# Performance work log

Hardware: AMD Instinct MI355X
Metric: run time of the kernel (lower is better)

Reference implementation:

```python
import jax, jax.numpy as jnp
import numpy as np

DIN = 1024
DOUT = 1024
NUM_HEAD = 16
HEAD_DIM = DIN // NUM_HEAD  # 64
SEQ = 2048
BS = 4


def setup_inputs() -> dict:
    key = jax.random.key(0)
    ks = jax.random.split(key, 9)
    s_in = 1.0 / np.sqrt(DIN)
    s_out = 1.0 / np.sqrt(DOUT)
    return {
        "x": jax.random.normal(ks[0], (BS, SEQ, DIN), dtype=jnp.float32),
        "Wq": jax.random.normal(ks[1], (DIN, DOUT), dtype=jnp.float32) * s_in,
        "bq": jax.random.normal(ks[2], (DOUT,), dtype=jnp.float32) * s_in,
        "Wk": jax.random.normal(ks[3], (DIN, DOUT), dtype=jnp.float32) * s_in,
        "bk": jax.random.normal(ks[4], (DOUT,), dtype=jnp.float32) * s_in,
        "Wv": jax.random.normal(ks[5], (DIN, DOUT), dtype=jnp.float32) * s_in,
        "bv": jax.random.normal(ks[6], (DOUT,), dtype=jnp.float32) * s_in,
        "Wo": jax.random.normal(ks[7], (DOUT, DOUT), dtype=jnp.float32) * s_out,
        "bo": jax.random.normal(ks[8], (DOUT,), dtype=jnp.float32) * s_out,
    }


def reference(x, Wq, bq, Wk, bk, Wv, bv, Wo, bo):
    bs, n, _ = x.shape
    # projections -> [bs, n, H, hd] -> [bs, H, n, hd]
    def split_heads(t):
        return t.reshape(bs, n, NUM_HEAD, HEAD_DIM).transpose(0, 2, 1, 3)

    q = split_heads(x @ Wq + bq)
    k = split_heads(x @ Wk + bk)
    v = split_heads(x @ Wv + bv)

    # full [bs, H, n, n] scores, causal mask, scaled softmax
    scores = jnp.einsum("bhqd,bhkd->bhqk", q, k)
    causal = jnp.tril(jnp.ones((n, n), dtype=bool))
    scores = jnp.where(causal, scores, -jnp.inf)
    att = jax.nn.softmax(scores / np.sqrt(HEAD_DIM), axis=-1)

    ctx = jnp.einsum("bhqk,bhkd->bhqd", att, v)
    ctx = ctx.transpose(0, 2, 1, 3).reshape(bs, n, DOUT)
    return ctx @ Wo + bo
```

## Files before the change

kernel.cpp:

```cpp
#include <hip/hip_runtime.h>
#include <hip/hip_bf16.h>
#include <stdint.h>

#define DIN   1024
#define DOUT  1024
#define NHEAD 16
#define HDIM  64
#define SEQL  2048
#define BSZ   4
#define MTOT  (BSZ*SEQL)
#define KDIM  1024

typedef __bf16 bf16x8 __attribute__((ext_vector_type(8)));
typedef float  f32x4  __attribute__((ext_vector_type(4)));

__device__ __forceinline__ f32x4 mfma16(bf16x8 a, bf16x8 b, f32x4 c) {
    return __builtin_amdgcn_mfma_f32_16x16x32_bf16(a, b, c, 0, 0, 0);
}

__device__ __forceinline__ void gl_lds16(const void* gsrc, void* ldst) {
    __builtin_amdgcn_global_load_lds(
        (const __attribute__((address_space(1))) uint32_t*)gsrc,
        (__attribute__((address_space(3))) uint32_t*)ldst, 16, 0, 0);
}

__device__ __forceinline__ unsigned short f2bf(float f) {
    union { __hip_bfloat16 h; unsigned short u; } cv;
    cv.h = __float2bfloat16(f);
    return cv.u;
}

__global__ void cvt_bf16(const float4* __restrict__ in, ushort4* __restrict__ out, int n4) {
    int idx = blockIdx.x * blockDim.x + threadIdx.x;
    int stride = gridDim.x * blockDim.x;
    for (int i = idx; i < n4; i += stride) {
        float4 v = in[i];
        ushort4 o;
        o.x = f2bf(v.x); o.y = f2bf(v.y); o.z = f2bf(v.z); o.w = f2bf(v.w);
        out[i] = o;
    }
}

__global__ void transpose_cvt3(const float* __restrict__ W0, const float* __restrict__ W1,
                               const float* __restrict__ W2, __hip_bfloat16* __restrict__ Wt3) {
    __shared__ __hip_bfloat16 t[32][33];
    const int tx = threadIdx.x, ty = threadIdx.y;
    const int bx = blockIdx.x, by = blockIdx.y, z = blockIdx.z;
    const float* W = (z == 0) ? W0 : (z == 1) ? W1 : W2;
    __hip_bfloat16* Wt = Wt3 + (size_t)z * DOUT * DIN;
#pragma unroll
    for (int r = 0; r < 4; ++r)
        t[ty + 8*r][tx] = __float2bfloat16(W[(size_t)(by*32 + ty + 8*r) * DOUT + bx*32 + tx]);
    __syncthreads();
#pragma unroll
    for (int r = 0; r < 4; ++r)
        Wt[(size_t)(bx*32 + ty + 8*r) * DIN + by*32 + tx] = t[tx][ty + 8*r];
}

__global__ void transpose_cvt(const float* __restrict__ W, __hip_bfloat16* __restrict__ Wt) {
    __shared__ __hip_bfloat16 t[32][33];
    const int tx = threadIdx.x, ty = threadIdx.y;
    const int bx = blockIdx.x, by = blockIdx.y;
#pragma unroll
    for (int r = 0; r < 4; ++r)
        t[ty + 8*r][tx] = __float2bfloat16(W[(size_t)(by*32 + ty + 8*r) * DOUT + bx*32 + tx]);
    __syncthreads();
#pragma unroll
    for (int r = 0; r < 4; ++r)
        Wt[(size_t)(bx*32 + ty + 8*r) * DIN + by*32 + tx] = t[tx][ty + 8*r];
}

template <int EPI>
__global__ __launch_bounds__(256)
void gemm_mfma(const __hip_bfloat16* __restrict__ A,
               const __hip_bfloat16* __restrict__ Bt,
               const float* __restrict__ b0, const float* __restrict__ b1,
               const float* __restrict__ b2,
               void* __restrict__ o0, void* __restrict__ o1, void* __restrict__ o2,
               float scale)
{
    __shared__ alignas(16) __hip_bfloat16 As[2][4][128][8];
    __shared__ alignas(16) __hip_bfloat16 Bs[2][4][128][8];

    const int tid  = threadIdx.x;
    const int w    = tid >> 6;
    const int lane = tid & 63;
    const int g    = lane >> 4;
    const int r    = lane & 15;
    const int wr   = w >> 1, wc = w & 1;

    const int row0 = blockIdx.y * 128;
    const int col0 = blockIdx.x * 128;

    f32x4 acc[4][4];
#pragma unroll
    for (int m = 0; m < 4; ++m)
#pragma unroll
        for (int n = 0; n < 4; ++n) acc[m][n] = (f32x4)0.0f;

    auto stage = [&](int buf, int kt) {
        const __hip_bfloat16* ga = A  + (size_t)(row0 + lane) * KDIM + kt*32 + 8*w;
        const __hip_bfloat16* gb = Bt + (size_t)(col0 + lane) * KDIM + kt*32 + 8*w;
        gl_lds16(ga,            &As[buf][w][0][0]);
        gl_lds16(ga + 64*KDIM,  &As[buf][w][64][0]);
        gl_lds16(gb,            &Bs[buf][w][0][0]);
        gl_lds16(gb + 64*KDIM,  &Bs[buf][w][64][0]);
    };

    stage(0, 0);
    __syncthreads();

    const int NKT = KDIM / 32;
    for (int kt = 0; kt < NKT; ++kt) {
        const int cur = kt & 1;
        if (kt + 1 < NKT) stage(cur ^ 1, kt + 1);

        bf16x8 af[4], bfr[4];
#pragma unroll
        for (int m = 0; m < 4; ++m)
            af[m] = *reinterpret_cast<const bf16x8*>(&As[cur][g][64*wr + 16*m + r][0]);
#pragma unroll
        for (int n = 0; n < 4; ++n)
            bfr[n] = *reinterpret_cast<const bf16x8*>(&Bs[cur][g][64*wc + 16*n + r][0]);

#pragma unroll
        for (int m = 0; m < 4; ++m)
#pragma unroll
            for (int n = 0; n < 4; ++n)
                acc[m][n] = mfma16(af[m], bfr[n], acc[m][n]);

        __syncthreads();
    }

#pragma unroll
    for (int n = 0; n < 4; ++n) {
        const int colg = col0 + 64*wc + 16*n + r;
        if (EPI == 2) {
            const float bv_ = b0[colg];
#pragma unroll
            for (int m = 0; m < 4; ++m) {
                const int rowg0 = row0 + 64*wr + 16*m + 4*g;
#pragma unroll
                for (int j = 0; j < 4; ++j)
                    ((float*)o0)[(size_t)(rowg0 + j) * DOUT + colg] = acc[m][n][j] + bv_;
            }
        } else {
            const int slab = colg >> 10;
            const int c2   = colg & 1023;
            const float* bp = (slab == 0) ? b0 : (slab == 1) ? b1 : b2;
            const float bv_ = bp[c2];
            const int hh = c2 >> 6, dd = c2 & (HDIM-1);
#pragma unroll
            for (int m = 0; m < 4; ++m) {
                const int rowg0 = row0 + 64*wr + 16*m + 4*g;
#pragma unroll
                for (int j = 0; j < 4; ++j) {
                    const int rowg = rowg0 + j;
                    const int bb = rowg >> 11, sq = rowg & (SEQL-1);
                    const float v = acc[m][n][j] + bv_;
                    if (slab == 0)
                        ((__hip_bfloat16*)o0)[(((size_t)(bb*NHEAD + hh) * SEQL + sq) << 6) + dd] =
                            __float2bfloat16(v * scale);
                    else if (slab == 1)
                        ((__hip_bfloat16*)o1)[(((size_t)(bb*NHEAD + hh) * SEQL + sq) << 6) + dd] =
                            __float2bfloat16(v);
                    else
                        ((__hip_bfloat16*)o2)[((size_t)(bb*NHEAD + hh) * HDIM + dd) * SEQL + sq] =
                            __float2bfloat16(v);
                }
            }
        }
    }
}

__global__ __launch_bounds__(256)
void attn_fwd(const __hip_bfloat16* __restrict__ Q,
              const __hip_bfloat16* __restrict__ K,
              const __hip_bfloat16* __restrict__ Vt,
              __hip_bfloat16* __restrict__ ctx)
{
    __shared__ alignas(16) __hip_bfloat16 Ps[4][2][16][64];

    const int tid  = threadIdx.x;
    const int w    = tid >> 6;
    const int lane = tid & 63;
    const int g    = lane >> 4;
    const int r    = lane & 15;
    const int swz  = (r & 7) << 3;

    const int bh = blockIdx.y;
    const int b  = bh >> 4, h = bh & 15;

    const __hip_bfloat16* Qh = Q  + (size_t)bh * SEQL * HDIM;
    const __hip_bfloat16* Kh = K  + (size_t)bh * SEQL * HDIM;
    const __hip_bfloat16* Vh = Vt + (size_t)bh * HDIM * SEQL;

    const int sp = blockIdx.x * 4 + w;

#pragma unroll 1
    for (int ti = 0; ti < 2; ++ti) {
        const int strip = ti ? (63 - sp) : sp;
        const int qb = strip * 32;

        bf16x8 qf[2][2];
#pragma unroll
        for (int m = 0; m < 2; ++m)
#pragma unroll
            for (int hh = 0; hh < 2; ++hh)
                qf[m][hh] = *reinterpret_cast<const bf16x8*>(
                    Qh + (size_t)(qb + 16*m + r) * HDIM + 32*hh + 8*g);

        f32x4 o[2][4];
        float mrow[2], lrow[2];
#pragma unroll
        for (int m = 0; m < 2; ++m) {
#pragma unroll
            for (int n = 0; n < 4; ++n) o[m][n] = (f32x4)0.0f;
            mrow[m] = -1e30f; lrow[m] = 0.0f;
        }

        const int nst = ((qb + 31) >> 6) + 1;
#pragma unroll 1
        for (int kt = 0; kt < nst; ++kt) {
            const int key0 = kt * 64;

            bf16x8 kf[4][2];
#pragma unroll
            for (int c = 0; c < 4; ++c)
#pragma unroll
                for (int hh = 0; hh < 2; ++hh)
                    kf[c][hh] = *reinterpret_cast<const bf16x8*>(
                        Kh + (size_t)(key0 + 16*c + r) * HDIM + 32*hh + 8*g);

            f32x4 s[2][4];
#pragma unroll
            for (int m = 0; m < 2; ++m)
#pragma unroll
                for (int c = 0; c < 4; ++c) {
                    f32x4 t = (f32x4)0.0f;
                    t = mfma16(kf[c][0], qf[m][0], t);
                    t = mfma16(kf[c][1], qf[m][1], t);
                    s[m][c] = t;
                }

            if (kt == nst - 1) {
#pragma unroll
                for (int m = 0; m < 2; ++m) {
                    const int qrow = qb + 16*m + r;
#pragma unroll
                    for (int c = 0; c < 4; ++c) {
                        const int kb = key0 + 16*c + 4*g;
#pragma unroll
                        for (int j = 0; j < 4; ++j)
                            if (kb + j > qrow) s[m][c][j] = -1e30f;
                    }
                }
            }

#pragma unroll
            for (int m = 0; m < 2; ++m) {
                float t0 = fmaxf(fmaxf(s[m][0][0], s[m][0][1]), fmaxf(s[m][0][2], s[m][0][3]));
                float t1 = fmaxf(fmaxf(s[m][1][0], s[m][1][1]), fmaxf(s[m][1][2], s[m][1][3]));
                float t2 = fmaxf(fmaxf(s[m][2][0], s[m][2][1]), fmaxf(s[m][2][2], s[m][2][3]));
                float t3 = fmaxf(fmaxf(s[m][3][0], s[m][3][1]), fmaxf(s[m][3][2], s[m][3][3]));
                float pm = fmaxf(fmaxf(t0, t1), fmaxf(t2, t3));
                pm = fmaxf(pm, __shfl_xor(pm, 16));
                pm = fmaxf(pm, __shfl_xor(pm, 32));

                if (__any(pm > mrow[m] + 11.0f)) {
                    const float mnew = fmaxf(mrow[m], pm);
                    const float fac  = exp2f(mrow[m] - mnew);
                    mrow[m] = mnew;
                    lrow[m] *= fac;
#pragma unroll
                    for (int n = 0; n < 4; ++n) o[m][n] *= fac;
                }

                float p[4][4];
#pragma unroll
                for (int c = 0; c < 4; ++c)
#pragma unroll
                    for (int j = 0; j < 4; ++j)
                        p[c][j] = exp2f(s[m][c][j] - mrow[m]);

                float u0 = (p[0][0] + p[0][1]) + (p[0][2] + p[0][3]);
                float u1 = (p[1][0] + p[1][1]) + (p[1][2] + p[1][3]);
                float u2 = (p[2][0] + p[2][1]) + (p[2][2] + p[2][3]);
                float u3 = (p[3][0] + p[3][1]) + (p[3][2] + p[3][3]);
                float ps = (u0 + u1) + (u2 + u3);
                ps += __shfl_xor(ps, 16);
                ps += __shfl_xor(ps, 32);
                lrow[m] += ps;

#pragma unroll
                for (int c = 0; c < 4; ++c) {
                    ushort4 pk4;
                    pk4.x = f2bf(p[c][0]); pk4.y = f2bf(p[c][1]);
                    pk4.z = f2bf(p[c][2]); pk4.w = f2bf(p[c][3]);
                    *reinterpret_cast<ushort4*>(&Ps[w][m][r][(16*c + 4*g) ^ swz]) = pk4;
                }
            }

            bf16x8 pf[2][2];
#pragma unroll
            for (int m = 0; m < 2; ++m)
#pragma unroll
                for (int hh = 0; hh < 2; ++hh)
                    pf[m][hh] = *reinterpret_cast<const bf16x8*>(
                        &Ps[w][m][r][(32*hh + 8*g) ^ swz]);

#pragma unroll
            for (int n = 0; n < 4; ++n) {
                bf16x8 vf0 = *reinterpret_cast<const bf16x8*>(
                    Vh + (size_t)(16*n + r) * SEQL + key0 + 8*g);
                bf16x8 vf1 = *reinterpret_cast<const bf16x8*>(
                    Vh + (size_t)(16*n + r) * SEQL + key0 + 32 + 8*g);
#pragma unroll
                for (int m = 0; m < 2; ++m) {
                    o[m][n] = mfma16(vf0, pf[m][0], o[m][n]);
                    o[m][n] = mfma16(vf1, pf[m][1], o[m][n]);
                }
            }
        }

#pragma unroll
        for (int m = 0; m < 2; ++m) {
            const float inv = 1.0f / lrow[m];
            const size_t rowbase = (size_t)(b*SEQL + qb + 16*m + r) * DOUT + h*HDIM;
#pragma unroll
            for (int n = 0; n < 4; ++n) {
                ushort4 ov;
                ov.x = f2bf(o[m][n][0] * inv); ov.y = f2bf(o[m][n][1] * inv);
                ov.z = f2bf(o[m][n][2] * inv); ov.w = f2bf(o[m][n][3] * inv);
                *reinterpret_cast<ushort4*>(&ctx[rowbase + 16*n + 4*g]) = ov;
            }
        }
    }
}

extern "C" void kernel_launch(void* const* d_in, const int* in_sizes, int n_in,
                              void* d_out, int out_size, void* d_ws, size_t ws_size,
                              hipStream_t stream) {
    const float* x  = (const float*)d_in[0];
    const float* Wq = (const float*)d_in[1];
    const float* bq = (const float*)d_in[2];
    const float* Wk = (const float*)d_in[3];
    const float* bk = (const float*)d_in[4];
    const float* Wv = (const float*)d_in[5];
    const float* bv = (const float*)d_in[6];
    const float* Wo = (const float*)d_in[7];
    const float* bo = (const float*)d_in[8];
    float* out = (float*)d_out;
    (void)in_sizes; (void)n_in; (void)out_size; (void)ws_size;

    char* ws = (char*)d_ws;
    __hip_bfloat16* xb  = (__hip_bfloat16*)ws;
    __hip_bfloat16* Wt3 = (__hip_bfloat16*)(ws + (16u << 20));
    __hip_bfloat16* Wot = (__hip_bfloat16*)(ws + (22u << 20));
    __hip_bfloat16* Qb  = (__hip_bfloat16*)(ws + (24u << 20));
    __hip_bfloat16* Kb  = Qb + (size_t)MTOT * DOUT;
    __hip_bfloat16* Vtb = Kb + (size_t)MTOT * DOUT;
    __hip_bfloat16* ctx = xb;

    cvt_bf16<<<2048, 256, 0, stream>>>((const float4*)x, (ushort4*)xb, MTOT * DIN / 4);

    dim3 tb(32, 8);
    transpose_cvt3<<<dim3(32, 32, 3), tb, 0, stream>>>(Wq, Wk, Wv, Wt3);
    transpose_cvt <<<dim3(32, 32),    tb, 0, stream>>>(Wo, Wot);

    dim3 gq(3*DOUT / 128, MTOT / 128);
    gemm_mfma<3><<<gq, 256, 0, stream>>>(xb, Wt3, bq, bk, bv, Qb, Kb, Vtb,
                                         0.125f * 1.44269504088896f);

    dim3 ag(8, BSZ * NHEAD);
    attn_fwd<<<ag, 256, 0, stream>>>(Qb, Kb, Vtb, ctx);

    dim3 gg(DOUT / 128, MTOT / 128);
    gemm_mfma<2><<<gg, 256, 0, stream>>>(ctx, Wot, bo, nullptr, nullptr,
                                         out, nullptr, nullptr, 1.0f);
}
```

Before: 316.1 us.

## Vectorize GEMM epilogues via operand swap, split V projection, shrink attention strips

The GEMM epilogues now swap MFMA operand order for the Q/K and output projections, so each lane holds four consecutive columns and can write them with one vector store and a float4 bias load. The V projection becomes its own launch whose epilogue writes the transposed V with ushort4 stores along the sequence dimension. The attention kernel drops from 32-row to 16-row query strips per wave and doubles the grid, which should balance the causal load better and use fewer registers. The cost is that K and V fragments are reloaded from global memory twice as often per query row, plus one extra kernel launch.

```diff
diff --git a/kernel.cpp b/kernel.cpp
--- a/kernel.cpp
+++ b/kernel.cpp
@@ -75,8 +75,7 @@
 void gemm_mfma(const __hip_bfloat16* __restrict__ A,
                const __hip_bfloat16* __restrict__ Bt,
                const float* __restrict__ b0, const float* __restrict__ b1,
-               const float* __restrict__ b2,
-               void* __restrict__ o0, void* __restrict__ o1, void* __restrict__ o2,
+               void* __restrict__ o0, void* __restrict__ o1,
                float scale)
 {
     __shared__ alignas(16) __hip_bfloat16 As[2][4][128][8];
@@ -126,48 +125,70 @@
 #pragma unroll
         for (int m = 0; m < 4; ++m)
 #pragma unroll
-            for (int n = 0; n < 4; ++n)
-                acc[m][n] = mfma16(af[m], bfr[n], acc[m][n]);
+            for (int n = 0; n < 4; ++n) {
+                if (EPI == 1) acc[m][n] = mfma16(af[m], bfr[n], acc[m][n]);
+                else          acc[m][n] = mfma16(bfr[n], af[m], acc[m][n]);
+            }
 
         __syncthreads();
     }
 
-#pragma unroll
-    for (int n = 0; n < 4; ++n) {
-        const int colg = col0 + 64*wc + 16*n + r;
-        if (EPI == 2) {
+    if (EPI == 0) {
+        const int slab = col0 >> 10;
+        const float* bp = (slab == 0) ? b0 : b1;
+        __hip_bfloat16* op = (__hip_bfloat16*)((slab == 0) ? o0 : o1);
+        const float sc = (slab == 0) ? scale : 1.0f;
+#pragma unroll
+        for (int m = 0; m < 4; ++m) {
+            const int rowg = row0 + 64*wr + 16*m + r;
+            const int bb = rowg >> 11, sq = rowg & (SEQL-1);
+#pragma unroll
+            for (int n = 0; n < 4; ++n) {
+                const int c2 = (col0 & 1023) + 64*wc + 16*n + 4*g;
+                const int hh = c2 >> 6, dd = c2 & (HDIM-1);
+                const float4 bv4 = *reinterpret_cast<const float4*>(&bp[c2]);
+                ushort4 ov;
+                ov.x = f2bf((acc[m][n][0] + bv4.x) * sc);
+                ov.y = f2bf((acc[m][n][1] + bv4.y) * sc);
+                ov.z = f2bf((acc[m][n][2] + bv4.z) * sc);
+                ov.w = f2bf((acc[m][n][3] + bv4.w) * sc);
+                *reinterpret_cast<ushort4*>(
+                    &op[(((size_t)(bb*NHEAD + hh) * SEQL + sq) << 6) + dd]) = ov;
+            }
+        }
+    } else if (EPI == 1) {
+#pragma unroll
+        for (int n = 0; n < 4; ++n) {
+            const int colg = col0 + 64*wc + 16*n + r;
+            const int hh = colg >> 6, dd = colg & (HDIM-1);
             const float bv_ = b0[colg];
 #pragma unroll
             for (int m = 0; m < 4; ++m) {
                 const int rowg0 = row0 + 64*wr + 16*m + 4*g;
-#pragma unroll
-                for (int j = 0; j < 4; ++j)
-                    ((float*)o0)[(size_t)(rowg0 + j) * DOUT + colg] = acc[m][n][j] + bv_;
-            }
-        } else {
-            const int slab = colg >> 10;
-            const int c2   = colg & 1023;
-            const float* bp = (slab == 0) ? b0 : (slab == 1) ? b1 : b2;
-            const float bv_ = bp[c2];
-            const int hh = c2 >> 6, dd = c2 & (HDIM-1);
-#pragma unroll
-            for (int m = 0; m < 4; ++m) {
-                const int rowg0 = row0 + 64*wr + 16*m + 4*g;
-#pragma unroll
-                for (int j = 0; j < 4; ++j) {
-                    const int rowg = rowg0 + j;
-                    const int bb = rowg >> 11, sq = rowg & (SEQL-1);
-                    const float v = acc[m][n][j] + bv_;
-                    if (slab == 0)
-                        ((__hip_bfloat16*)o0)[(((size_t)(bb*NHEAD + hh) * SEQL + sq) << 6) + dd] =
-                            __float2bfloat16(v * scale);
-                    else if (slab == 1)
-                        ((__hip_bfloat16*)o1)[(((size_t)(bb*NHEAD + hh) * SEQL + sq) << 6) + dd] =
-                            __float2bfloat16(v);
-                    else
-                        ((__hip_bfloat16*)o2)[((size_t)(bb*NHEAD + hh) * HDIM + dd) * SEQL + sq] =
-                            __float2bfloat16(v);
-                }
+                const int bb = rowg0 >> 11, sq0 = rowg0 & (SEQL-1);
+                ushort4 ov;
+                ov.x = f2bf(acc[m][n][0] + bv_);
+                ov.y = f2bf(acc[m][n][1] + bv_);
+                ov.z = f2bf(acc[m][n][2] + bv_);
+                ov.w = f2bf(acc[m][n][3] + bv_);
+                *reinterpret_cast<ushort4*>(
+                    &((__hip_bfloat16*)o0)[((size_t)(bb*NHEAD + hh) * HDIM + dd) * SEQL + sq0]) = ov;
+            }
+        }
+    } else {
+#pragma unroll
+        for (int m = 0; m < 4; ++m) {
+            const int rowg = row0 + 64*wr + 16*m + r;
+#pragma unroll
+            for (int n = 0; n < 4; ++n) {
+                const int colg0 = col0 + 64*wc + 16*n + 4*g;
+                const float4 bv4 = *reinterpret_cast<const float4*>(&b0[colg0]);
+                float4 ov;
+                ov.x = acc[m][n][0] + bv4.x;
+                ov.y = acc[m][n][1] + bv4.y;
+                ov.z = acc[m][n][2] + bv4.z;
+                ov.w = acc[m][n][3] + bv4.w;
+                *reinterpret_cast<float4*>(&((float*)o0)[(size_t)rowg * DOUT + colg0]) = ov;
             }
         }
     }
@@ -179,7 +200,7 @@
               const __hip_bfloat16* __restrict__ Vt,
               __hip_bfloat16* __restrict__ ctx)
 {
-    __shared__ alignas(16) __hip_bfloat16 Ps[4][2][16][64];
+    __shared__ alignas(16) __hip_bfloat16 Ps[4][16][64];
 
     const int tid  = threadIdx.x;
     const int w    = tid >> 6;
@@ -199,27 +220,22 @@
 
 #pragma unroll 1
     for (int ti = 0; ti < 2; ++ti) {
-        const int strip = ti ? (63 - sp) : sp;
-        const int qb = strip * 32;
-
-        bf16x8 qf[2][2];
-#pragma unroll
-        for (int m = 0; m < 2; ++m)
-#pragma unroll
-            for (int hh = 0; hh < 2; ++hh)
-                qf[m][hh] = *reinterpret_cast<const bf16x8*>(
-                    Qh + (size_t)(qb + 16*m + r) * HDIM + 32*hh + 8*g);
-
-        f32x4 o[2][4];
-        float mrow[2], lrow[2];
-#pragma unroll
-        for (int m = 0; m < 2; ++m) {
-#pragma unroll
-            for (int n = 0; n < 4; ++n) o[m][n] = (f32x4)0.0f;
-            mrow[m] = -1e30f; lrow[m] = 0.0f;
-        }
-
-        const int nst = ((qb + 31) >> 6) + 1;
+        const int strip = ti ? (127 - sp) : sp;
+        const int qb = strip * 16;
+        const int qrow = qb + r;
+
+        bf16x8 qf[2];
+#pragma unroll
+        for (int hh = 0; hh < 2; ++hh)
+            qf[hh] = *reinterpret_cast<const bf16x8*>(
+                Qh + (size_t)qrow * HDIM + 32*hh + 8*g);
+
+        f32x4 o[4];
+#pragma unroll
+        for (int n = 0; n < 4; ++n) o[n] = (f32x4)0.0f;
+        float mrow = -1e30f, lrow = 0.0f;
+
+        const int nst = (qb >> 6) + 1;
 #pragma unroll 1
         for (int kt = 0; kt < nst; ++kt) {
             const int key0 = kt * 64;
@@ -232,82 +248,71 @@
                     kf[c][hh] = *reinterpret_cast<const bf16x8*>(
                         Kh + (size_t)(key0 + 16*c + r) * HDIM + 32*hh + 8*g);
 
-            f32x4 s[2][4];
-#pragma unroll
-            for (int m = 0; m < 2; ++m)
+            f32x4 s[4];
+#pragma unroll
+            for (int c = 0; c < 4; ++c) {
+                f32x4 t = (f32x4)0.0f;
+                t = mfma16(kf[c][0], qf[0], t);
+                t = mfma16(kf[c][1], qf[1], t);
+                s[c] = t;
+            }
+
+            if (kt == nst - 1) {
 #pragma unroll
                 for (int c = 0; c < 4; ++c) {
-                    f32x4 t = (f32x4)0.0f;
-                    t = mfma16(kf[c][0], qf[m][0], t);
-                    t = mfma16(kf[c][1], qf[m][1], t);
-                    s[m][c] = t;
+                    const int kb = key0 + 16*c + 4*g;
+#pragma unroll
+                    for (int j = 0; j < 4; ++j)
+                        if (kb + j > qrow) s[c][j] = -1e30f;
                 }
-
-            if (kt == nst - 1) {
-#pragma unroll
-                for (int m = 0; m < 2; ++m) {
-                    const int qrow = qb + 16*m + r;
-#pragma unroll
-                    for (int c = 0; c < 4; ++c) {
-                        const int kb = key0 + 16*c + 4*g;
-#pragma unroll
-                        for (int j = 0; j < 4; ++j)
-                            if (kb + j > qrow) s[m][c][j] = -1e30f;
-                    }
-                }
-            }
-
-#pragma unroll
-            for (int m = 0; m < 2; ++m) {
-                float t0 = fmaxf(fmaxf(s[m][0][0], s[m][0][1]), fmaxf(s[m][0][2], s[m][0][3]));
-                float t1 = fmaxf(fmaxf(s[m][1][0], s[m][1][1]), fmaxf(s[m][1][2], s[m][1][3]));
-                float t2 = fmaxf(fmaxf(s[m][2][0], s[m][2][1]), fmaxf(s[m][2][2], s[m][2][3]));
-                float t3 = fmaxf(fmaxf(s[m][3][0], s[m][3][1]), fmaxf(s[m][3][2], s[m][3][3]));
-                float pm = fmaxf(fmaxf(t0, t1), fmaxf(t2, t3));
-                pm = fmaxf(pm, __shfl_xor(pm, 16));
-                pm = fmaxf(pm, __shfl_xor(pm, 32));
-
-                if (__any(pm > mrow[m] + 11.0f)) {
-                    const float mnew = fmaxf(mrow[m], pm);
-                    const float fac  = exp2f(mrow[m] - mnew);
-                    mrow[m] = mnew;
-                    lrow[m] *= fac;
-#pragma unroll
-                    for (int n = 0; n < 4; ++n) o[m][n] *= fac;
-                }
-
-                float p[4][4];
-#pragma unroll
-                for (int c = 0; c < 4; ++c)
-#pragma unroll
-                    for (int j = 0; j < 4; ++j)
-                        p[c][j] = exp2f(s[m][c][j] - mrow[m]);
-
-                float u0 = (p[0][0] + p[0][1]) + (p[0][2] + p[0][3]);
-                float u1 = (p[1][0] + p[1][1]) + (p[1][2] + p[1][3]);
-                float u2 = (p[2][0] + p[2][1]) + (p[2][2] + p[2][3]);
-                float u3 = (p[3][0] + p[3][1]) + (p[3][2] + p[3][3]);
-                float ps = (u0 + u1) + (u2 + u3);
-                ps += __shfl_xor(ps, 16);
-                ps += __shfl_xor(ps, 32);
-                lrow[m] += ps;
-
-#pragma unroll
-                for (int c = 0; c < 4; ++c) {
-                    ushort4 pk4;
-                    pk4.x = f2bf(p[c][0]); pk4.y = f2bf(p[c][1]);
-                    pk4.z = f2bf(p[c][2]); pk4.w = f2bf(p[c][3]);
-                    *reinterpret_cast<ushort4*>(&Ps[w][m][r][(16*c + 4*g) ^ swz]) = pk4;
-                }
-            }
-
-            bf16x8 pf[2][2];
-#pragma unroll
-            for (int m = 0; m < 2; ++m)
-#pragma unroll
-                for (int hh = 0; hh < 2; ++hh)
-                    pf[m][hh] = *reinterpret_cast<const bf16x8*>(
-                        &Ps[w][m][r][(32*hh + 8*g) ^ swz]);
+            }
+
+            float t0 = fmaxf(fmaxf(s[0][0], s[0][1]), fmaxf(s[0][2], s[0][3]));
+            float t1 = fmaxf(fmaxf(s[1][0], s[1][1]), fmaxf(s[1][2], s[1][3]));
+            float t2 = fmaxf(fmaxf(s[2][0], s[2][1]), fmaxf(s[2][2], s[2][3]));
+            float t3 = fmaxf(fmaxf(s[3][0], s[3][1]), fmaxf(s[3][2], s[3][3]));
+            float pm = fmaxf(fmaxf(t0, t1), fmaxf(t2, t3));
+            pm = fmaxf(pm, __shfl_xor(pm, 16));
+            pm = fmaxf(pm, __shfl_xor(pm, 32));
+
+            if (__any(pm > mrow + 11.0f)) {
+                const float mnew = fmaxf(mrow, pm);
+                const float fac  = exp2f(mrow - mnew);
+                mrow = mnew;
+                lrow *= fac;
+#pragma unroll
+                for (int n = 0; n < 4; ++n) o[n] *= fac;
+            }
+
+            float p[4][4];
+#pragma unroll
+            for (int c = 0; c < 4; ++c)
+#pragma unroll
+                for (int j = 0; j < 4; ++j)
+                    p[c][j] = exp2f(s[c][j] - mrow);
+
+            float u0 = (p[0][0] + p[0][1]) + (p[0][2] + p[0][3]);
+            float u1 = (p[1][0] + p[1][1]) + (p[1][2] + p[1][3]);
+            float u2 = (p[2][0] + p[2][1]) + (p[2][2] + p[2][3]);
+            float u3 = (p[3][0] + p[3][1]) + (p[3][2] + p[3][3]);
+            float ps = (u0 + u1) + (u2 + u3);
+            ps += __shfl_xor(ps, 16);
+            ps += __shfl_xor(ps, 32);
+            lrow += ps;
+
+#pragma unroll
+            for (int c = 0; c < 4; ++c) {
+                ushort4 pk4;
+                pk4.x = f2bf(p[c][0]); pk4.y = f2bf(p[c][1]);
+                pk4.z = f2bf(p[c][2]); pk4.w = f2bf(p[c][3]);
+                *reinterpret_cast<ushort4*>(&Ps[w][r][(16*c + 4*g) ^ swz]) = pk4;
+            }
+
+            bf16x8 pf[2];
+#pragma unroll
+            for (int hh = 0; hh < 2; ++hh)
+                pf[hh] = *reinterpret_cast<const bf16x8*>(
+                    &Ps[w][r][(32*hh + 8*g) ^ swz]);
 
 #pragma unroll
             for (int n = 0; n < 4; ++n) {
@@ -315,25 +320,19 @@
                     Vh + (size_t)(16*n + r) * SEQL + key0 + 8*g);
                 bf16x8 vf1 = *reinterpret_cast<const bf16x8*>(
                     Vh + (size_t)(16*n + r) * SEQL + key0 + 32 + 8*g);
-#pragma unroll
-                for (int m = 0; m < 2; ++m) {
-                    o[m][n] = mfma16(vf0, pf[m][0], o[m][n]);
-                    o[m][n] = mfma16(vf1, pf[m][1], o[m][n]);
-                }
-            }
-        }
-
-#pragma unroll
-        for (int m = 0; m < 2; ++m) {
-            const float inv = 1.0f / lrow[m];
-            const size_t rowbase = (size_t)(b*SEQL + qb + 16*m + r) * DOUT + h*HDIM;
-#pragma unroll
-            for (int n = 0; n < 4; ++n) {
-                ushort4 ov;
-                ov.x = f2bf(o[m][n][0] * inv); ov.y = f2bf(o[m][n][1] * inv);
-                ov.z = f2bf(o[m][n][2] * inv); ov.w = f2bf(o[m][n][3] * inv);
-                *reinterpret_cast<ushort4*>(&ctx[rowbase + 16*n + 4*g]) = ov;
-            }
+                o[n] = mfma16(vf0, pf[0], o[n]);
+                o[n] = mfma16(vf1, pf[1], o[n]);
+            }
+        }
+
+        const float inv = 1.0f / lrow;
+        const size_t rowbase = (size_t)(b*SEQL + qrow) * DOUT + h*HDIM;
+#pragma unroll
+        for (int n = 0; n < 4; ++n) {
+            ushort4 ov;
+            ov.x = f2bf(o[n][0] * inv); ov.y = f2bf(o[n][1] * inv);
+            ov.z = f2bf(o[n][2] * inv); ov.w = f2bf(o[n][3] * inv);
+            *reinterpret_cast<ushort4*>(&ctx[rowbase + 16*n + 4*g]) = ov;
         }
     }
 }
@@ -368,14 +367,16 @@
     transpose_cvt3<<<dim3(32, 32, 3), tb, 0, stream>>>(Wq, Wk, Wv, Wt3);
     transpose_cvt <<<dim3(32, 32),    tb, 0, stream>>>(Wo, Wot);
 
-    dim3 gq(3*DOUT / 128, MTOT / 128);
-    gemm_mfma<3><<<gq, 256, 0, stream>>>(xb, Wt3, bq, bk, bv, Qb, Kb, Vtb,
-                                         0.125f * 1.44269504088896f);
-
-    dim3 ag(8, BSZ * NHEAD);
+    dim3 gqk(2*DOUT / 128, MTOT / 128);
+    gemm_mfma<0><<<gqk, 256, 0, stream>>>(xb, Wt3, bq, bk, Qb, Kb,
+                                          0.125f * 1.44269504088896f);
+    dim3 gv(DOUT / 128, MTOT / 128);
+    gemm_mfma<1><<<gv, 256, 0, stream>>>(xb, Wt3 + (size_t)2*DOUT*DIN, bv, nullptr,
+                                         Vtb, nullptr, 1.0f);
+
+    dim3 ag(16, BSZ * NHEAD);
     attn_fwd<<<ag, 256, 0, stream>>>(Qb, Kb, Vtb, ctx);
 
-    dim3 gg(DOUT / 128, MTOT / 128);
-    gemm_mfma<2><<<gg, 256, 0, stream>>>(ctx, Wot, bo, nullptr, nullptr,
-                                         out, nullptr, nullptr, 1.0f);
-}
+    gemm_mfma<2><<<gv, 256, 0, stream>>>(ctx, Wot, bo, nullptr,
+                                         out, nullptr, 1.0f);
+}
```

New measurement: 414.2 us. 1.31x slower.

## Use 256x256 tiles for QKV GEMM and vectorize epilogues via operand swap

Applied to the files above, without the earlier changes.

The fused QKV projection moves from 128x128 tiles with 256 threads to 256x256 tiles with 512 threads (8 waves, launch_bounds 512,2), which raises arithmetic intensity per LDS load. For Q/K slabs and for the output GEMM, the MFMA operands are swapped so each lane holds four consecutive columns, allowing packed ushort4/float4 stores and float4 bias loads instead of scalar strided writes. The V slab keeps the original operand order so its transposed layout can be written as four consecutive sequence positions. The larger tile raises register pressure and reduces grid size to 12x32 blocks, which can hurt occupancy or load balance.

```diff
diff --git a/kernel.cpp b/kernel.cpp
--- a/kernel.cpp
+++ b/kernel.cpp
@@ -70,14 +70,130 @@
         Wt[(size_t)(bx*32 + ty + 8*r) * DIN + by*32 + tx] = t[tx][ty + 8*r];
 }
 
-template <int EPI>
+__global__ __launch_bounds__(512, 2)
+void gemm_qkv256(const __hip_bfloat16* __restrict__ A,
+                 const __hip_bfloat16* __restrict__ Bt,
+                 const float* __restrict__ bq, const float* __restrict__ bk,
+                 const float* __restrict__ bv,
+                 __hip_bfloat16* __restrict__ Qo, __hip_bfloat16* __restrict__ Ko,
+                 __hip_bfloat16* __restrict__ Vo,
+                 float qscale)
+{
+    __shared__ alignas(16) __hip_bfloat16 As[2][4][256][8];
+    __shared__ alignas(16) __hip_bfloat16 Bs[2][4][256][8];
+
+    const int tid  = threadIdx.x;
+    const int w    = tid >> 6;
+    const int lane = tid & 63;
+    const int g    = lane >> 4;
+    const int r    = lane & 15;
+    const int wr   = w >> 2;
+    const int wc   = w & 3;
+    const int sg   = w & 3;
+    const int sb   = w >> 2;
+
+    const int row0 = blockIdx.y * 256;
+    const int col0 = blockIdx.x * 256;
+    const bool vslab = (col0 >= 2048);
+
+    f32x4 acc[8][4];
+#pragma unroll
+    for (int m = 0; m < 8; ++m)
+#pragma unroll
+        for (int n = 0; n < 4; ++n) acc[m][n] = (f32x4)0.0f;
+
+    auto stage = [&](int buf, int kt) {
+        const __hip_bfloat16* ga = A  + (size_t)(row0 + sb*128 + lane) * KDIM + kt*32 + 8*sg;
+        const __hip_bfloat16* gb = Bt + (size_t)(col0 + sb*128 + lane) * KDIM + kt*32 + 8*sg;
+        gl_lds16(ga,           &As[buf][sg][sb*128     ][0]);
+        gl_lds16(ga + 64*KDIM, &As[buf][sg][sb*128 + 64][0]);
+        gl_lds16(gb,           &Bs[buf][sg][sb*128     ][0]);
+        gl_lds16(gb + 64*KDIM, &Bs[buf][sg][sb*128 + 64][0]);
+    };
+
+    stage(0, 0);
+    __syncthreads();
+
+    const int NKT = KDIM / 32;
+    for (int kt = 0; kt < NKT; ++kt) {
+        const int cur = kt & 1;
+        if (kt + 1 < NKT) stage(cur ^ 1, kt + 1);
+
+        bf16x8 af[8], bfr[4];
+#pragma unroll
+        for (int m = 0; m < 8; ++m)
+            af[m] = *reinterpret_cast<const bf16x8*>(&As[cur][g][wr*128 + 16*m + r][0]);
+#pragma unroll
+        for (int n = 0; n < 4; ++n)
+            bfr[n] = *reinterpret_cast<const bf16x8*>(&Bs[cur][g][wc*64 + 16*n + r][0]);
+
+        if (!vslab) {
+#pragma unroll
+            for (int m = 0; m < 8; ++m)
+#pragma unroll
+                for (int n = 0; n < 4; ++n)
+                    acc[m][n] = mfma16(bfr[n], af[m], acc[m][n]);
+        } else {
+#pragma unroll
+            for (int m = 0; m < 8; ++m)
+#pragma unroll
+                for (int n = 0; n < 4; ++n)
+                    acc[m][n] = mfma16(af[m], bfr[n], acc[m][n]);
+        }
+
+        __syncthreads();
+    }
+
+    if (!vslab) {
+        const int slab = col0 >> 10;
+        const float* bp = (slab == 0) ? bq : bk;
+        __hip_bfloat16* op = (slab == 0) ? Qo : Ko;
+        const float sc = (slab == 0) ? qscale : 1.0f;
+#pragma unroll
+        for (int m = 0; m < 8; ++m) {
+            const int rowg = row0 + wr*128 + 16*m + r;
+            const int bb = rowg >> 11, sq = rowg & (SEQL-1);
+#pragma unroll
+            for (int n = 0; n < 4; ++n) {
+                const int c2 = (col0 & 1023) + wc*64 + 16*n + 4*g;
+                const int hh = c2 >> 6, dd = c2 & (HDIM-1);
+                const float4 bv4 = *reinterpret_cast<const float4*>(&bp[c2]);
+                ushort4 ov;
+                ov.x = f2bf((acc[m][n][0] + bv4.x) * sc);
+                ov.y = f2bf((acc[m][n][1] + bv4.y) * sc);
+                ov.z = f2bf((acc[m][n][2] + bv4.z) * sc);
+                ov.w = f2bf((acc[m][n][3] + bv4.w) * sc);
+                *reinterpret_cast<ushort4*>(
+                    &op[(((size_t)(bb*NHEAD + hh) * SEQL + sq) << 6) + dd]) = ov;
+            }
+        }
+    } else {
+#pragma unroll
+        for (int n = 0; n < 4; ++n) {
+            const int colg = (col0 - 2048) + wc*64 + 16*n + r;
+            const int hh = colg >> 6, dd = colg & (HDIM-1);
+            const float bvv = bv[colg];
+#pragma unroll
+            for (int m = 0; m < 8; ++m) {
+                const int rowg0 = row0 + wr*128 + 16*m + 4*g;
+                const int bb = rowg0 >> 11, sq0 = rowg0 & (SEQL-1);
+                ushort4 ov;
+                ov.x = f2bf(acc[m][n][0] + bvv);
+                ov.y = f2bf(acc[m][n][1] + bvv);
+                ov.z = f2bf(acc[m][n][2] + bvv);
+                ov.w = f2bf(acc[m][n][3] + bvv);
+                *reinterpret_cast<ushort4*>(
+                    &Vo[((size_t)(bb*NHEAD + hh) * HDIM + dd) * SEQL + sq0]) = ov;
+            }
+        }
+    }
+}
+
 __global__ __launch_bounds__(256)
-void gemm_mfma(const __hip_bfloat16* __restrict__ A,
-               const __hip_bfloat16* __restrict__ Bt,
-               const float* __restrict__ b0, const float* __restrict__ b1,
-               const float* __restrict__ b2,
-               void* __restrict__ o0, void* __restrict__ o1, void* __restrict__ o2,
-               float scale)
+void gemm_out128(const __hip_bfloat16* __restrict__ A,
+                 const __hip_bfloat16* __restrict__ Bt,
+                 const float* __restrict__ b0,
+                 float* __restrict__ o0)
 {
     __shared__ alignas(16) __hip_bfloat16 As[2][4][128][8];
     __shared__ alignas(16) __hip_bfloat16 Bs[2][4][128][8];
@@ -127,48 +243,24 @@
         for (int m = 0; m < 4; ++m)
 #pragma unroll
             for (int n = 0; n < 4; ++n)
-                acc[m][n] = mfma16(af[m], bfr[n], acc[m][n]);
+                acc[m][n] = mfma16(bfr[n], af[m], acc[m][n]);
 
         __syncthreads();
     }
 
 #pragma unroll
-    for (int n = 0; n < 4; ++n) {
-        const int colg = col0 + 64*wc + 16*n + r;
-        if (EPI == 2) {
-            const float bv_ = b0[colg];
-#pragma unroll
-            for (int m = 0; m < 4; ++m) {
-                const int rowg0 = row0 + 64*wr + 16*m + 4*g;
-#pragma unroll
-                for (int j = 0; j < 4; ++j)
-                    ((float*)o0)[(size_t)(rowg0 + j) * DOUT + colg] = acc[m][n][j] + bv_;
-            }
-        } else {
-            const int slab = colg >> 10;
-            const int c2   = colg & 1023;
-            const float* bp = (slab == 0) ? b0 : (slab == 1) ? b1 : b2;
-            const float bv_ = bp[c2];
-            const int hh = c2 >> 6, dd = c2 & (HDIM-1);
-#pragma unroll
-            for (int m = 0; m < 4; ++m) {
-                const int rowg0 = row0 + 64*wr + 16*m + 4*g;
-#pragma unroll
-                for (int j = 0; j < 4; ++j) {
-                    const int rowg = rowg0 + j;
-                    const int bb = rowg >> 11, sq = rowg & (SEQL-1);
-                    const float v = acc[m][n][j] + bv_;
-                    if (slab == 0)
-                        ((__hip_bfloat16*)o0)[(((size_t)(bb*NHEAD + hh) * SEQL + sq) << 6) + dd] =
-                            __float2bfloat16(v * scale);
-                    else if (slab == 1)
-                        ((__hip_bfloat16*)o1)[(((size_t)(bb*NHEAD + hh) * SEQL + sq) << 6) + dd] =
-                            __float2bfloat16(v);
-                    else
-                        ((__hip_bfloat16*)o2)[((size_t)(bb*NHEAD + hh) * HDIM + dd) * SEQL + sq] =
-                            __float2bfloat16(v);
-                }
-            }
+    for (int m = 0; m < 4; ++m) {
+        const int rowg = row0 + 64*wr + 16*m + r;
+#pragma unroll
+        for (int n = 0; n < 4; ++n) {
+            const int colg0 = col0 + 64*wc + 16*n + 4*g;
+            const float4 bv4 = *reinterpret_cast<const float4*>(&b0[colg0]);
+            float4 ov;
+            ov.x = acc[m][n][0] + bv4.x;
+            ov.y = acc[m][n][1] + bv4.y;
+            ov.z = acc[m][n][2] + bv4.z;
+            ov.w = acc[m][n][3] + bv4.w;
+            *reinterpret_cast<float4*>(&o0[(size_t)rowg * DOUT + colg0]) = ov;
         }
     }
 }
@@ -368,14 +460,13 @@
     transpose_cvt3<<<dim3(32, 32, 3), tb, 0, stream>>>(Wq, Wk, Wv, Wt3);
     transpose_cvt <<<dim3(32, 32),    tb, 0, stream>>>(Wo, Wot);
 
-    dim3 gq(3*DOUT / 128, MTOT / 128);
-    gemm_mfma<3><<<gq, 256, 0, stream>>>(xb, Wt3, bq, bk, bv, Qb, Kb, Vtb,
-                                         0.125f * 1.44269504088896f);
+    dim3 gq(3*DOUT / 256, MTOT / 256);
+    gemm_qkv256<<<gq, 512, 0, stream>>>(xb, Wt3, bq, bk, bv, Qb, Kb, Vtb,
+                                        0.125f * 1.44269504088896f);
 
     dim3 ag(8, BSZ * NHEAD);
     attn_fwd<<<ag, 256, 0, stream>>>(Qb, Kb, Vtb, ctx);
 
     dim3 gg(DOUT / 128, MTOT / 128);
-    gemm_mfma<2><<<gg, 256, 0, stream>>>(ctx, Wot, bo, nullptr, nullptr,
-                                         out, nullptr, nullptr, 1.0f);
-}
+    gemm_out128<<<gg, 256, 0, stream>>>(ctx, Wot, bo, out);
+}
```

Result: slower. 671.4 us (+112.4%).

## Vectorize GEMM epilogues via operand swap and split QKV launch, one strip per wave

Applied to the files above, without the earlier changes.

The GEMM epilogues now swap the MFMA operands for the Q/K and output projections so each lane holds four consecutive columns, which allows vectorized ushort4/float4 stores and float4 bias loads. The V projection gets its own launch that keeps the original operand order so that the transposed V store writes four consecutive sequence positions per lane. Attention launches twice as many blocks, with each wave handling one query strip instead of a balanced pair. The intent is to cut scattered scalar stores and to raise attention parallelism. The cost is an extra launch and less even per-wave work in attention.

```diff
diff --git a/kernel.cpp b/kernel.cpp
--- a/kernel.cpp
+++ b/kernel.cpp
@@ -75,8 +75,7 @@
 void gemm_mfma(const __hip_bfloat16* __restrict__ A,
                const __hip_bfloat16* __restrict__ Bt,
                const float* __restrict__ b0, const float* __restrict__ b1,
-               const float* __restrict__ b2,
-               void* __restrict__ o0, void* __restrict__ o1, void* __restrict__ o2,
+               void* __restrict__ o0, void* __restrict__ o1,
                float scale)
 {
     __shared__ alignas(16) __hip_bfloat16 As[2][4][128][8];
@@ -126,48 +125,70 @@
 #pragma unroll
         for (int m = 0; m < 4; ++m)
 #pragma unroll
-            for (int n = 0; n < 4; ++n)
-                acc[m][n] = mfma16(af[m], bfr[n], acc[m][n]);
+            for (int n = 0; n < 4; ++n) {
+                if (EPI == 1) acc[m][n] = mfma16(af[m], bfr[n], acc[m][n]);
+                else          acc[m][n] = mfma16(bfr[n], af[m], acc[m][n]);
+            }
 
         __syncthreads();
     }
 
-#pragma unroll
-    for (int n = 0; n < 4; ++n) {
-        const int colg = col0 + 64*wc + 16*n + r;
-        if (EPI == 2) {
+    if (EPI == 0) {
+        const int slab = col0 >> 10;
+        const float* bp = (slab == 0) ? b0 : b1;
+        __hip_bfloat16* op = (__hip_bfloat16*)((slab == 0) ? o0 : o1);
+        const float sc = (slab == 0) ? scale : 1.0f;
+#pragma unroll
+        for (int m = 0; m < 4; ++m) {
+            const int rowg = row0 + 64*wr + 16*m + r;
+            const int bb = rowg >> 11, sq = rowg & (SEQL-1);
+#pragma unroll
+            for (int n = 0; n < 4; ++n) {
+                const int c2 = (col0 & 1023) + 64*wc + 16*n + 4*g;
+                const int hh = c2 >> 6, dd = c2 & (HDIM-1);
+                const float4 bv4 = *reinterpret_cast<const float4*>(&bp[c2]);
+                ushort4 ov;
+                ov.x = f2bf((acc[m][n][0] + bv4.x) * sc);
+                ov.y = f2bf((acc[m][n][1] + bv4.y) * sc);
+                ov.z = f2bf((acc[m][n][2] + bv4.z) * sc);
+                ov.w = f2bf((acc[m][n][3] + bv4.w) * sc);
+                *reinterpret_cast<ushort4*>(
+                    &op[(((size_t)(bb*NHEAD + hh) * SEQL + sq) << 6) + dd]) = ov;
+            }
+        }
+    } else if (EPI == 1) {
+#pragma unroll
+        for (int n = 0; n < 4; ++n) {
+            const int colg = col0 + 64*wc + 16*n + r;
+            const int hh = colg >> 6, dd = colg & (HDIM-1);
             const float bv_ = b0[colg];
 #pragma unroll
             for (int m = 0; m < 4; ++m) {
                 const int rowg0 = row0 + 64*wr + 16*m + 4*g;
-#pragma unroll
-                for (int j = 0; j < 4; ++j)
-                    ((float*)o0)[(size_t)(rowg0 + j) * DOUT + colg] = acc[m][n][j] + bv_;
-            }
-        } else {
-            const int slab = colg >> 10;
-            const int c2   = colg & 1023;
-            const float* bp = (slab == 0) ? b0 : (slab == 1) ? b1 : b2;
-            const float bv_ = bp[c2];
-            const int hh = c2 >> 6, dd = c2 & (HDIM-1);
-#pragma unroll
-            for (int m = 0; m < 4; ++m) {
-                const int rowg0 = row0 + 64*wr + 16*m + 4*g;
-#pragma unroll
-                for (int j = 0; j < 4; ++j) {
-                    const int rowg = rowg0 + j;
-                    const int bb = rowg >> 11, sq = rowg & (SEQL-1);
-                    const float v = acc[m][n][j] + bv_;
-                    if (slab == 0)
-                        ((__hip_bfloat16*)o0)[(((size_t)(bb*NHEAD + hh) * SEQL + sq) << 6) + dd] =
-                            __float2bfloat16(v * scale);
-                    else if (slab == 1)
-                        ((__hip_bfloat16*)o1)[(((size_t)(bb*NHEAD + hh) * SEQL + sq) << 6) + dd] =
-                            __float2bfloat16(v);
-                    else
-                        ((__hip_bfloat16*)o2)[((size_t)(bb*NHEAD + hh) * HDIM + dd) * SEQL + sq] =
-                            __float2bfloat16(v);
-                }
+                const int bb = rowg0 >> 11, sq0 = rowg0 & (SEQL-1);
+                ushort4 ov;
+                ov.x = f2bf(acc[m][n][0] + bv_);
+                ov.y = f2bf(acc[m][n][1] + bv_);
+                ov.z = f2bf(acc[m][n][2] + bv_);
+                ov.w = f2bf(acc[m][n][3] + bv_);
+                *reinterpret_cast<ushort4*>(
+                    &((__hip_bfloat16*)o0)[((size_t)(bb*NHEAD + hh) * HDIM + dd) * SEQL + sq0]) = ov;
+            }
+        }
+    } else {
+#pragma unroll
+        for (int m = 0; m < 4; ++m) {
+            const int rowg = row0 + 64*wr + 16*m + r;
+#pragma unroll
+            for (int n = 0; n < 4; ++n) {
+                const int colg0 = col0 + 64*wc + 16*n + 4*g;
+                const float4 bv4 = *reinterpret_cast<const float4*>(&b0[colg0]);
+                float4 ov;
+                ov.x = acc[m][n][0] + bv4.x;
+                ov.y = acc[m][n][1] + bv4.y;
+                ov.z = acc[m][n][2] + bv4.z;
+                ov.w = acc[m][n][3] + bv4.w;
+                *reinterpret_cast<float4*>(&((float*)o0)[(size_t)rowg * DOUT + colg0]) = ov;
             }
         }
     }
@@ -195,145 +216,141 @@
     const __hip_bfloat16* Kh = K  + (size_t)bh * SEQL * HDIM;
     const __hip_bfloat16* Vh = Vt + (size_t)bh * HDIM * SEQL;
 
-    const int sp = blockIdx.x * 4 + w;
-
+    const int gsp   = blockIdx.x * 4 + w;
+    const int strip = 63 - gsp;
+    const int qb    = strip * 32;
+
+    bf16x8 qf[2][2];
+#pragma unroll
+    for (int m = 0; m < 2; ++m)
+#pragma unroll
+        for (int hh = 0; hh < 2; ++hh)
+            qf[m][hh] = *reinterpret_cast<const bf16x8*>(
+                Qh + (size_t)(qb + 16*m + r) * HDIM + 32*hh + 8*g);
+
+    f32x4 o[2][4];
+    float mrow[2], lrow[2];
+#pragma unroll
+    for (int m = 0; m < 2; ++m) {
+#pragma unroll
+        for (int n = 0; n < 4; ++n) o[m][n] = (f32x4)0.0f;
+        mrow[m] = -1e30f; lrow[m] = 0.0f;
+    }
+
+    const int nst = ((qb + 31) >> 6) + 1;
 #pragma unroll 1
-    for (int ti = 0; ti < 2; ++ti) {
-        const int strip = ti ? (63 - sp) : sp;
-        const int qb = strip * 32;
-
-        bf16x8 qf[2][2];
+    for (int kt = 0; kt < nst; ++kt) {
+        const int key0 = kt * 64;
+
+        bf16x8 kf[4][2];
+#pragma unroll
+        for (int c = 0; c < 4; ++c)
+#pragma unroll
+            for (int hh = 0; hh < 2; ++hh)
+                kf[c][hh] = *reinterpret_cast<const bf16x8*>(
+                    Kh + (size_t)(key0 + 16*c + r) * HDIM + 32*hh + 8*g);
+
+        f32x4 s[2][4];
 #pragma unroll
         for (int m = 0; m < 2; ++m)
 #pragma unroll
+            for (int c = 0; c < 4; ++c) {
+                f32x4 t = (f32x4)0.0f;
+                t = mfma16(kf[c][0], qf[m][0], t);
+                t = mfma16(kf[c][1], qf[m][1], t);
+                s[m][c] = t;
+            }
+
+        if (kt == nst - 1) {
+#pragma unroll
+            for (int m = 0; m < 2; ++m) {
+                const int qrow = qb + 16*m + r;
+#pragma unroll
+                for (int c = 0; c < 4; ++c) {
+                    const int kb = key0 + 16*c + 4*g;
+#pragma unroll
+                    for (int j = 0; j < 4; ++j)
+                        if (kb + j > qrow) s[m][c][j] = -1e30f;
+                }
+            }
+        }
+
+#pragma unroll
+        for (int m = 0; m < 2; ++m) {
+            float t0 = fmaxf(fmaxf(s[m][0][0], s[m][0][1]), fmaxf(s[m][0][2], s[m][0][3]));
+            float t1 = fmaxf(fmaxf(s[m][1][0], s[m][1][1]), fmaxf(s[m][1][2], s[m][1][3]));
+            float t2 = fmaxf(fmaxf(s[m][2][0], s[m][2][1]), fmaxf(s[m][2][2], s[m][2][3]));
+            float t3 = fmaxf(fmaxf(s[m][3][0], s[m][3][1]), fmaxf(s[m][3][2], s[m][3][3]));
+            float pm = fmaxf(fmaxf(t0, t1), fmaxf(t2, t3));
+            pm = fmaxf(pm, __shfl_xor(pm, 16));
+            pm = fmaxf(pm, __shfl_xor(pm, 32));
+
+            if (__any(pm > mrow[m] + 11.0f)) {
+                const float mnew = fmaxf(mrow[m], pm);
+                const float fac  = exp2f(mrow[m] - mnew);
+                mrow[m] = mnew;
+                lrow[m] *= fac;
+#pragma unroll
+                for (int n = 0; n < 4; ++n) o[m][n] *= fac;
+            }
+
+            float p[4][4];
+#pragma unroll
+            for (int c = 0; c < 4; ++c)
+#pragma unroll
+                for (int j = 0; j < 4; ++j)
+                    p[c][j] = exp2f(s[m][c][j] - mrow[m]);
+
+            float u0 = (p[0][0] + p[0][1]) + (p[0][2] + p[0][3]);
+            float u1 = (p[1][0] + p[1][1]) + (p[1][2] + p[1][3]);
+            float u2 = (p[2][0] + p[2][1]) + (p[2][2] + p[2][3]);
+            float u3 = (p[3][0] + p[3][1]) + (p[3][2] + p[3][3]);
+            float ps = (u0 + u1) + (u2 + u3);
+            ps += __shfl_xor(ps, 16);
+            ps += __shfl_xor(ps, 32);
+            lrow[m] += ps;
+
+#pragma unroll
+            for (int c = 0; c < 4; ++c) {
+                ushort4 pk4;
+                pk4.x = f2bf(p[c][0]); pk4.y = f2bf(p[c][1]);
+                pk4.z = f2bf(p[c][2]); pk4.w = f2bf(p[c][3]);
+                *reinterpret_cast<ushort4*>(&Ps[w][m][r][(16*c + 4*g) ^ swz]) = pk4;
+            }
+        }
+
+        bf16x8 pf[2][2];
+#pragma unroll
+        for (int m = 0; m < 2; ++m)
+#pragma unroll
             for (int hh = 0; hh < 2; ++hh)
-                qf[m][hh] = *reinterpret_cast<const bf16x8*>(
-                    Qh + (size_t)(qb + 16*m + r) * HDIM + 32*hh + 8*g);
-
-        f32x4 o[2][4];
-        float mrow[2], lrow[2];
-#pragma unroll
-        for (int m = 0; m < 2; ++m) {
-#pragma unroll
-            for (int n = 0; n < 4; ++n) o[m][n] = (f32x4)0.0f;
-            mrow[m] = -1e30f; lrow[m] = 0.0f;
-        }
-
-        const int nst = ((qb + 31) >> 6) + 1;
-#pragma unroll 1
-        for (int kt = 0; kt < nst; ++kt) {
-            const int key0 = kt * 64;
-
-            bf16x8 kf[4][2];
-#pragma unroll
-            for (int c = 0; c < 4; ++c)
-#pragma unroll
-                for (int hh = 0; hh < 2; ++hh)
-                    kf[c][hh] = *reinterpret_cast<const bf16x8*>(
-                        Kh + (size_t)(key0 + 16*c + r) * HDIM + 32*hh + 8*g);
-
-            f32x4 s[2][4];
-#pragma unroll
-            for (int m = 0; m < 2; ++m)
-#pragma unroll
-                for (int c = 0; c < 4; ++c) {
-                    f32x4 t = (f32x4)0.0f;
-                    t = mfma16(kf[c][0], qf[m][0], t);
-                    t = mfma16(kf[c][1], qf[m][1], t);
-                    s[m][c] = t;
-                }
-
-            if (kt == nst - 1) {
-#pragma unroll
-                for (int m = 0; m < 2; ++m) {
-                    const int qrow = qb + 16*m + r;
-#pragma unroll
-                    for (int c = 0; c < 4; ++c) {
-                        const int kb = key0 + 16*c + 4*g;
-#pragma unroll
-                        for (int j = 0; j < 4; ++j)
-                            if (kb + j > qrow) s[m][c][j] = -1e30f;
-                    }
-                }
-            }
-
+                pf[m][hh] = *reinterpret_cast<const bf16x8*>(
+                    &Ps[w][m][r][(32*hh + 8*g) ^ swz]);
+
+#pragma unroll
+        for (int n = 0; n < 4; ++n) {
+            bf16x8 vf0 = *reinterpret_cast<const bf16x8*>(
+                Vh + (size_t)(16*n + r) * SEQL + key0 + 8*g);
+            bf16x8 vf1 = *reinterpret_cast<const bf16x8*>(
+                Vh + (size_t)(16*n + r) * SEQL + key0 + 32 + 8*g);
 #pragma unroll
             for (int m = 0; m < 2; ++m) {
-                float t0 = fmaxf(fmaxf(s[m][0][0], s[m][0][1]), fmaxf(s[m][0][2], s[m][0][3]));
-                float t1 = fmaxf(fmaxf(s[m][1][0], s[m][1][1]), fmaxf(s[m][1][2], s[m][1][3]));
-                float t2 = fmaxf(fmaxf(s[m][2][0], s[m][2][1]), fmaxf(s[m][2][2], s[m][2][3]));
-                float t3 = fmaxf(fmaxf(s[m][3][0], s[m][3][1]), fmaxf(s[m][3][2], s[m][3][3]));
-                float pm = fmaxf(fmaxf(t0, t1), fmaxf(t2, t3));
-                pm = fmaxf(pm, __shfl_xor(pm, 16));
-                pm = fmaxf(pm, __shfl_xor(pm, 32));
-
-                if (__any(pm > mrow[m] + 11.0f)) {
-                    const float mnew = fmaxf(mrow[m], pm);
-                    const float fac  = exp2f(mrow[m] - mnew);
-                    mrow[m] = mnew;
-                    lrow[m] *= fac;
-#pragma unroll
-                    for (int n = 0; n < 4; ++n) o[m][n] *= fac;
-                }
-
-                float p[4][4];
-#pragma unroll
-                for (int c = 0; c < 4; ++c)
-#pragma unroll
-                    for (int j = 0; j < 4; ++j)
-                        p[c][j] = exp2f(s[m][c][j] - mrow[m]);
-
-                float u0 = (p[0][0] + p[0][1]) + (p[0][2] + p[0][3]);
-                float u1 = (p[1][0] + p[1][1]) + (p[1][2] + p[1][3]);
-                float u2 = (p[2][0] + p[2][1]) + (p[2][2] + p[2][3]);
-                float u3 = (p[3][0] + p[3][1]) + (p[3][2] + p[3][3]);
-                float ps = (u0 + u1) + (u2 + u3);
-                ps += __shfl_xor(ps, 16);
-                ps += __shfl_xor(ps, 32);
-                lrow[m] += ps;
-
-#pragma unroll
-                for (int c = 0; c < 4; ++c) {
-                    ushort4 pk4;
-                    pk4.x = f2bf(p[c][0]); pk4.y = f2bf(p[c][1]);
-                    pk4.z = f2bf(p[c][2]); pk4.w = f2bf(p[c][3]);
-                    *reinterpret_cast<ushort4*>(&Ps[w][m][r][(16*c + 4*g) ^ swz]) = pk4;
-                }
-            }
-
-            bf16x8 pf[2][2];
-#pragma unroll
-            for (int m = 0; m < 2; ++m)
-#pragma unroll
-                for (int hh = 0; hh < 2; ++hh)
-                    pf[m][hh] = *reinterpret_cast<const bf16x8*>(
-                        &Ps[w][m][r][(32*hh + 8*g) ^ swz]);
-
-#pragma unroll
-            for (int n = 0; n < 4; ++n) {
-                bf16x8 vf0 = *reinterpret_cast<const bf16x8*>(
-                    Vh + (size_t)(16*n + r) * SEQL + key0 + 8*g);
-                bf16x8 vf1 = *reinterpret_cast<const bf16x8*>(
-                    Vh + (size_t)(16*n + r) * SEQL + key0 + 32 + 8*g);
-#pragma unroll
-                for (int m = 0; m < 2; ++m) {
-                    o[m][n] = mfma16(vf0, pf[m][0], o[m][n]);
-                    o[m][n] = mfma16(vf1, pf[m][1], o[m][n]);
-                }
-            }
-        }
-
-#pragma unroll
-        for (int m = 0; m < 2; ++m) {
-            const float inv = 1.0f / lrow[m];
-            const size_t rowbase = (size_t)(b*SEQL + qb + 16*m + r) * DOUT + h*HDIM;
-#pragma unroll
-            for (int n = 0; n < 4; ++n) {
-                ushort4 ov;
-                ov.x = f2bf(o[m][n][0] * inv); ov.y = f2bf(o[m][n][1] * inv);
-                ov.z = f2bf(o[m][n][2] * inv); ov.w = f2bf(o[m][n][3] * inv);
-                *reinterpret_cast<ushort4*>(&ctx[rowbase + 16*n + 4*g]) = ov;
-            }
+                o[m][n] = mfma16(vf0, pf[m][0], o[m][n]);
+                o[m][n] = mfma16(vf1, pf[m][1], o[m][n]);
+            }
+        }
+    }
+
+#pragma unroll
+    for (int m = 0; m < 2; ++m) {
+        const float inv = 1.0f / lrow[m];
+        const size_t rowbase = (size_t)(b*SEQL + qb + 16*m + r) * DOUT + h*HDIM;
+#pragma unroll
+        for (int n = 0; n < 4; ++n) {
+            ushort4 ov;
+            ov.x = f2bf(o[m][n][0] * inv); ov.y = f2bf(o[m][n][1] * inv);
+            ov.z = f2bf(o[m][n][2] * inv); ov.w = f2bf(o[m][n][3] * inv);
+            *reinterpret_cast<ushort4*>(&ctx[rowbase + 16*n + 4*g]) = ov;
         }
     }
 }
@@ -368,14 +385,16 @@
     transpose_cvt3<<<dim3(32, 32, 3), tb, 0, stream>>>(Wq, Wk, Wv, Wt3);
     transpose_cvt <<<dim3(32, 32),    tb, 0, stream>>>(Wo, Wot);
 
-    dim3 gq(3*DOUT / 128, MTOT / 128);
-    gemm_mfma<3><<<gq, 256, 0, stream>>>(xb, Wt3, bq, bk, bv, Qb, Kb, Vtb,
-                                         0.125f * 1.44269504088896f);
-
-    dim3 ag(8, BSZ * NHEAD);
+    dim3 gqk(2*DOUT / 128, MTOT / 128);
+    gemm_mfma<0><<<gqk, 256, 0, stream>>>(xb, Wt3, bq, bk, Qb, Kb,
+                                          0.125f * 1.44269504088896f);
+    dim3 gv(DOUT / 128, MTOT / 128);
+    gemm_mfma<1><<<gv, 256, 0, stream>>>(xb, Wt3 + (size_t)2*DOUT*DIN, bv, nullptr,
+                                         Vtb, nullptr, 1.0f);
+
+    dim3 ag(16, BSZ * NHEAD);
     attn_fwd<<<ag, 256, 0, stream>>>(Qb, Kb, Vtb, ctx);
 
-    dim3 gg(DOUT / 128, MTOT / 128);
-    gemm_mfma<2><<<gg, 256, 0, stream>>>(ctx, Wot, bo, nullptr, nullptr,
-                                         out, nullptr, nullptr, 1.0f);
-}
+    gemm_mfma<2><<<gv, 256, 0, stream>>>(ctx, Wot, bo, nullptr,
+                                         out, nullptr, 1.0f);
+}
```

Measured after the change: 412.3 us. +30.5%, slower.
